# Kernel optimization log

Hardware: AMD Instinct MI355X
Metric: run time of the kernel (lower is better)

Reference implementation:

```python
import jax, jax.numpy as jnp
import numpy as np

N = 30000      # nodes
E = 480000     # edges (before self loops)
NFEAT = 128
H = 16         # heads
C = 32         # per-head channels = nhid
NCLASS = 10
G = 64         # graphs in batch
ATT_SLOPE = 0.2   # GATv2Conv negative_slope default
ACT_SLOPE = 0.01  # F.leaky_relu default


def setup_inputs() -> dict:
    key = jax.random.key(0)
    ks = jax.random.split(key, 16)
    def glorot(k, shape):
        fan = sum(shape[:2]) if len(shape) > 1 else shape[0]
        return jax.random.normal(k, shape, jnp.float32) * (2.0 / fan) ** 0.5
    inp = {
        "x": jax.random.normal(ks[0], (N, NFEAT), jnp.float32),
        # layer 1: lin_l / lin_r map NFEAT -> H*C, attention vector att [H, C]
        "Wl1": glorot(ks[1], (NFEAT, H * C)), "bl1": jnp.zeros((H * C,), jnp.float32),
        "Wr1": glorot(ks[2], (NFEAT, H * C)), "br1": jnp.zeros((H * C,), jnp.float32),
        "att1": glorot(ks[3], (H, C)), "b1": jnp.zeros((C,), jnp.float32),
        # layer 2: nhid(=C) -> H*C
        "Wl2": glorot(ks[4], (C, H * C)), "bl2": jnp.zeros((H * C,), jnp.float32),
        "Wr2": glorot(ks[5], (C, H * C)), "br2": jnp.zeros((H * C,), jnp.float32),
        "att2": glorot(ks[6], (H, C)), "b2": jnp.zeros((C,), jnp.float32),
        # classifier nhid -> nclass
        "Wc": glorot(ks[7], (C, NCLASS)), "bc": jnp.zeros((NCLASS,), jnp.float32),
        "edge_index": jax.random.randint(ks[8], (2, E), 0, N, jnp.int32),
        "batch": jnp.sort(jax.random.randint(ks[9], (N,), 0, G, jnp.int32)),
    }
    return inp


def _gatv2_layer(x, Wl, bl, Wr, br, att, b, src, dst, n):
    # GATv2Conv, concat=False (mean over heads), eval mode (no dropout)
    xl = (x @ Wl + bl).reshape(n, H, C)   # messages (x_j)
    xr = (x @ Wr + br).reshape(n, H, C)   # query side (x_i)
    e = jax.nn.leaky_relu(xl[src] + xr[dst], ATT_SLOPE)      # [E', H, C]
    score = jnp.einsum('ehc,hc->eh', e, att)                 # [E', H]
    # segment softmax over incoming edges of each dst node
    m = jax.ops.segment_max(score, dst, num_segments=n)
    ex = jnp.exp(score - m[dst])
    denom = jax.ops.segment_sum(ex, dst, num_segments=n)
    alpha = ex / denom[dst]                                  # [E', H]
    out = jax.ops.segment_sum(alpha[:, :, None] * xl[src], dst, num_segments=n)
    return out.mean(axis=1) + b                              # [n, C]


def reference(x, Wl1, bl1, Wr1, br1, att1, b1, Wl2, bl2, Wr2, br2, att2, b2, Wc, bc, edge_index, batch):
    # add self loops (PyG GATv2Conv default add_self_loops=True)
    loop = jnp.arange(N, dtype=edge_index.dtype)
    src = jnp.concatenate([edge_index[0], loop])
    dst = jnp.concatenate([edge_index[1], loop])

    h = jax.nn.leaky_relu(_gatv2_layer(x, Wl1, bl1, Wr1, br1, att1, b1, src, dst, N), ACT_SLOPE)
    h = jax.nn.leaky_relu(_gatv2_layer(h, Wl2, bl2, Wr2, br2, att2, b2, src, dst, N), ACT_SLOPE)
    # dropout is identity in eval mode
    # global mean pool over graphs
    summed = jax.ops.segment_sum(h, batch, num_segments=G)               # [G, C]
    counts = jax.ops.segment_sum(jnp.ones((N,), h.dtype), batch, num_segments=G)
    pooled = summed / jnp.maximum(counts, 1.0)[:, None]
    logits = pooled @ Wc + bc
    return logits / 1.0  # temperature = 1.0
```

## Files before the change

### kernel.cpp

```cpp
#include <hip/hip_runtime.h>
#include <float.h>

#define NNODES 30000
#define NEDGES 480000
#define NFEATK 128
#define NH 16
#define NC 32
#define HC 512
#define NCLASSES 10
#define NG 64
#define CAP 96

using half2v = __attribute__((ext_vector_type(2))) _Float16;
using half4 = __attribute__((ext_vector_type(4))) _Float16;
using half8 = __attribute__((ext_vector_type(8))) _Float16;
using f32x4 = __attribute__((ext_vector_type(4))) float;

__global__ void prep0_kernel(const float* __restrict__ x, _Float16* __restrict__ xh,
                             const float* __restrict__ Wl1, const float* __restrict__ Wr1,
                             _Float16* __restrict__ Wlt1, _Float16* __restrict__ Wrt1,
                             const float* __restrict__ Wl2, const float* __restrict__ Wr2,
                             _Float16* __restrict__ Wlt2, _Float16* __restrict__ Wrt2,
                             int* __restrict__ cnt, int* __restrict__ csr) {
    int gtid = blockIdx.x * blockDim.x + threadIdx.x;
    int gstride = gridDim.x * blockDim.x;
    for (int i = gtid; i < NNODES * NFEATK / 4; i += gstride) {
        float4 v = *(const float4*)&x[i * 4];
        half4 h = {(_Float16)v.x, (_Float16)v.y, (_Float16)v.z, (_Float16)v.w};
        *(half4*)&xh[i * 4] = h;
    }
    for (int i = gtid; i < 2 * 512 * NFEATK; i += gstride) {
        int sel = i >= 512 * NFEATK;
        int idx = i - sel * 512 * NFEATK;
        const float* W = sel ? Wr1 : Wl1;
        _Float16* Wt = sel ? Wrt1 : Wlt1;
        int n = idx & 511, k = idx >> 9;
        Wt[n * NFEATK + k] = (_Float16)W[idx];
    }
    for (int i = gtid; i < 2 * 512 * NC; i += gstride) {
        int sel = i >= 512 * NC;
        int idx = i - sel * 512 * NC;
        const float* W = sel ? Wr2 : Wl2;
        _Float16* Wt = sel ? Wrt2 : Wlt2;
        int n = idx & 511, k = idx >> 9;
        Wt[n * NC + k] = (_Float16)W[idx];
    }
    for (int i = gtid; i < NNODES; i += gstride) {
        cnt[i] = 1;
        csr[i * CAP] = i;
    }
}

__global__ void scatter_kernel(const int* __restrict__ src, const int* __restrict__ dst,
                               int* __restrict__ cnt, int* __restrict__ csr) {
    int e = blockIdx.x * blockDim.x + threadIdx.x;
    if (e >= NEDGES) return;
    int s = src[e], d = dst[e];
    int pos = atomicAdd(&cnt[d], 1);
    csr[d * CAP + pos] = s;
}

template <int K>
__launch_bounds__(256)
__global__ void dual_gemm_kernel(const _Float16* __restrict__ A,
                                 const _Float16* __restrict__ Wlt, const _Float16* __restrict__ Wrt,
                                 const float* __restrict__ bl, const float* __restrict__ br,
                                 _Float16* __restrict__ Yl, _Float16* __restrict__ Yr) {
    constexpr int Kc = K / 8;
    constexpr int AH = 64 * K;
    constexpr int BH = 128 * K;
    constexpr int YSH = 64 * 136;
    constexpr int SMEMH = (AH + BH > YSH) ? (AH + BH) : YSH;
    __shared__ __align__(16) _Float16 smem[SMEMH];
    _Float16* as = smem;
    _Float16* bs = smem + AH;

    int tid = threadIdx.x;
    int sel = blockIdx.y >> 2;
    int nbase = (blockIdx.y & 3) * 128;
    const _Float16* Bt = sel ? Wrt : Wlt;
    const float* bias = sel ? br : bl;
    _Float16* Y = sel ? Yr : Yl;
    int mb = blockIdx.x;

    for (int c = tid; c < 64 * Kc; c += 256) {
        int row = c / Kc, k8 = c % Kc;
        int arow = mb * 64 + row; if (arow > NNODES - 1) arow = NNODES - 1;
        half8 v = *(const half8*)&A[(size_t)arow * K + k8 * 8];
        *(half8*)&as[(row * Kc + (k8 ^ (row & (Kc - 1)))) * 8] = v;
    }
    for (int c = tid; c < 128 * Kc; c += 256) {
        int row = c / Kc, k8 = c % Kc;
        half8 v = *(const half8*)&Bt[(size_t)(nbase + row) * K + k8 * 8];
        *(half8*)&bs[(row * Kc + (k8 ^ (row & (Kc - 1)))) * 8] = v;
    }
    __syncthreads();

    int wave = tid >> 6, lane = tid & 63;
    int quad = lane >> 4, l16 = lane & 15;
    int am = l16 & (Kc - 1);

    f32x4 acc[8];
    #pragma unroll
    for (int f = 0; f < 8; f++) acc[f] = (f32x4){0.f, 0.f, 0.f, 0.f};

    #pragma unroll
    for (int kk = 0; kk < Kc; kk += 4) {
        int k8 = (kk + quad) ^ am;
        half8 a = *(const half8*)&as[((wave * 16 + l16) * Kc + k8) * 8];
        #pragma unroll
        for (int f = 0; f < 8; f++) {
            half8 b = *(const half8*)&bs[((f * 16 + l16) * Kc + k8) * 8];
            acc[f] = __builtin_amdgcn_mfma_f32_16x16x32_f16(a, b, acc[f], 0, 0, 0);
        }
    }
    __syncthreads();

    _Float16* ys = smem;
    #pragma unroll
    for (int f = 0; f < 8; f++) {
        float bv = bias[nbase + f * 16 + l16];
        #pragma unroll
        for (int r = 0; r < 4; r++) {
            ys[(wave * 16 + quad * 4 + r) * 136 + f * 16 + l16] = (_Float16)(acc[f][r] + bv);
        }
    }
    __syncthreads();
    int mtop = mb * 64;
    for (int c = tid; c < 64 * 16; c += 256) {
        int r = c >> 4, cc = (c & 15) * 8;
        int grow = mtop + r;
        if (grow < NNODES)
            *(half8*)&Y[(size_t)grow * HC + nbase + cc] = *(half8*)&ys[r * 136 + cc];
    }
}

__device__ inline half2v lrelu2(half2v e) {
    half2v s = e * half2v{(_Float16)0.2f, (_Float16)0.2f};
    return __builtin_elementwise_max(e, s);
}

#if __has_builtin(__builtin_amdgcn_fdot2)
#define FDOT2(a, b, c) __builtin_amdgcn_fdot2((a), (b), (c), false)
#else
__device__ inline float fdot2_sw(half2v a, half2v b, float c) {
    half2v p = a * b;
    return c + (float)p.x + (float)p.y;
}
#define FDOT2(a, b, c) fdot2_sw((a), (b), (c))
#endif

template <typename OUT>
__launch_bounds__(256)
__global__ void gat_edge_kernel(const _Float16* __restrict__ xlh, const _Float16* __restrict__ xrh,
                                const float* __restrict__ att, const float* __restrict__ bvec,
                                const int* __restrict__ cnt, const int* __restrict__ csr_src,
                                OUT* __restrict__ hout) {
    int wv = threadIdx.x >> 6;
    int t = threadIdx.x & 63;
    int d = blockIdx.x * 4 + wv;
    int col = t * 8;

    half8 xrq = *(const half8*)&xrh[(size_t)d * HC + col];
    half2v xr0 = {xrq[0], xrq[1]}, xr1 = {xrq[2], xrq[3]};
    half2v xr2 = {xrq[4], xrq[5]}, xr3 = {xrq[6], xrq[7]};
    float4 atta = *(const float4*)&att[col];
    float4 attb = *(const float4*)&att[col + 4];
    half2v at0 = {(_Float16)atta.x, (_Float16)atta.y};
    half2v at1 = {(_Float16)atta.z, (_Float16)atta.w};
    half2v at2 = {(_Float16)attb.x, (_Float16)attb.y};
    half2v at3 = {(_Float16)attb.z, (_Float16)attb.w};

    int beg = d * CAP, end = beg + cnt[d];

    float l = 0.f;
    float a[8];
    #pragma unroll
    for (int c = 0; c < 8; c++) a[c] = 0.f;

    for (int i = beg; i < end; i += 4) {
        int n = end - i;
        int s0 = csr_src[i];
        int s1 = csr_src[n > 1 ? i + 1 : i];
        int s2 = csr_src[n > 2 ? i + 2 : i];
        int s3 = csr_src[n > 3 ? i + 3 : i];
        half8 q0 = *(const half8*)&xlh[(size_t)s0 * HC + col];
        half8 q1 = *(const half8*)&xlh[(size_t)s1 * HC + col];
        half8 q2 = *(const half8*)&xlh[(size_t)s2 * HC + col];
        half8 q3 = *(const half8*)&xlh[(size_t)s3 * HC + col];

        float v0 = 0.f, v1 = 0.f, v2 = 0.f, v3 = 0.f;
        v0 = FDOT2(lrelu2(half2v{q0[0], q0[1]} + xr0), at0, v0);
        v0 = FDOT2(lrelu2(half2v{q0[2], q0[3]} + xr1), at1, v0);
        v0 = FDOT2(lrelu2(half2v{q0[4], q0[5]} + xr2), at2, v0);
        v0 = FDOT2(lrelu2(half2v{q0[6], q0[7]} + xr3), at3, v0);
        v1 = FDOT2(lrelu2(half2v{q1[0], q1[1]} + xr0), at0, v1);
        v1 = FDOT2(lrelu2(half2v{q1[2], q1[3]} + xr1), at1, v1);
        v1 = FDOT2(lrelu2(half2v{q1[4], q1[5]} + xr2), at2, v1);
        v1 = FDOT2(lrelu2(half2v{q1[6], q1[7]} + xr3), at3, v1);
        v2 = FDOT2(lrelu2(half2v{q2[0], q2[1]} + xr0), at0, v2);
        v2 = FDOT2(lrelu2(half2v{q2[2], q2[3]} + xr1), at1, v2);
        v2 = FDOT2(lrelu2(half2v{q2[4], q2[5]} + xr2), at2, v2);
        v2 = FDOT2(lrelu2(half2v{q2[6], q2[7]} + xr3), at3, v2);
        v3 = FDOT2(lrelu2(half2v{q3[0], q3[1]} + xr0), at0, v3);
        v3 = FDOT2(lrelu2(half2v{q3[2], q3[3]} + xr1), at1, v3);
        v3 = FDOT2(lrelu2(half2v{q3[4], q3[5]} + xr2), at2, v3);
        v3 = FDOT2(lrelu2(half2v{q3[6], q3[7]} + xr3), at3, v3);

        v0 += __shfl_xor(v0, 1); v1 += __shfl_xor(v1, 1);
        v2 += __shfl_xor(v2, 1); v3 += __shfl_xor(v3, 1);
        v0 += __shfl_xor(v0, 2); v1 += __shfl_xor(v1, 2);
        v2 += __shfl_xor(v2, 2); v3 += __shfl_xor(v3, 2);

        float p0 = __expf(v0);
        float p1 = (n > 1) ? __expf(v1) : 0.f;
        float p2 = (n > 2) ? __expf(v2) : 0.f;
        float p3 = (n > 3) ? __expf(v3) : 0.f;
        l += (p0 + p1) + (p2 + p3);

        #pragma unroll
        for (int c = 0; c < 8; c++) {
            a[c] += p0 * (float)q0[c];
            a[c] += p1 * (float)q1[c];
            a[c] += p2 * (float)q2[c];
            a[c] += p3 * (float)q3[c];
        }
    }

    float inv = 1.0f / l;
    #pragma unroll
    for (int c = 0; c < 8; c++) a[c] *= inv;

    #pragma unroll
    for (int off = 4; off < 64; off <<= 1) {
        #pragma unroll
        for (int c = 0; c < 8; c++) a[c] += __shfl_xor(a[c], off);
    }

    if (t < 4) {
        #pragma unroll
        for (int c = 0; c < 8; c++) {
            float r = a[c] * (1.0f / (float)NH) + bvec[t * 8 + c];
            r = (r > 0.f) ? r : 0.01f * r;
            hout[(size_t)d * NC + t * 8 + c] = (OUT)r;
        }
    }
}

__launch_bounds__(1024)
__global__ void pool_classify_kernel(const float* __restrict__ h, const int* __restrict__ batch,
                                     const float* __restrict__ Wc, const float* __restrict__ bc,
                                     float* __restrict__ out) {
    int g = blockIdx.x;
    int lo = 0, hi = NNODES;
    while (lo < hi) { int mid = (lo + hi) >> 1; if (batch[mid] < g) lo = mid + 1; else hi = mid; }
    int start = lo;
    hi = NNODES;
    while (lo < hi) { int mid = (lo + hi) >> 1; if (batch[mid] <= g) lo = mid + 1; else hi = mid; }
    int endn = lo;
    int cntg = endn - start;

    int tid = threadIdx.x;
    int c = tid & 31, nl = tid >> 5;
    float s = 0.f;
    for (int n = start + nl; n < endn; n += 32) s += h[n * NC + c];
    __shared__ float red[1024];
    red[tid] = s;
    __syncthreads();
    if (tid < 32) {
        float t = 0.f;
        #pragma unroll
        for (int j = 0; j < 32; j++) t += red[j * 32 + tid];
        red[tid] = t / fmaxf((float)cntg, 1.0f);
    }
    __syncthreads();
    if (tid < NCLASSES) {
        float sum = bc[tid];
        #pragma unroll
        for (int cc = 0; cc < NC; cc++) sum += red[cc] * Wc[cc * NCLASSES + tid];
        out[g * NCLASSES + tid] = sum;
    }
}


extern "C" void kernel_launch(void* const* d_in, const int* in_sizes, int n_in,
                              void* d_out, int out_size, void* d_ws, size_t ws_size,
                              hipStream_t stream) {
    const float* x    = (const float*)d_in[0];
    const float* Wl1  = (const float*)d_in[1];
    const float* bl1  = (const float*)d_in[2];
    const float* Wr1  = (const float*)d_in[3];
    const float* br1  = (const float*)d_in[4];
    const float* att1 = (const float*)d_in[5];
    const float* b1   = (const float*)d_in[6];
    const float* Wl2  = (const float*)d_in[7];
    const float* bl2  = (const float*)d_in[8];
    const float* Wr2  = (const float*)d_in[9];
    const float* br2  = (const float*)d_in[10];
    const float* att2 = (const float*)d_in[11];
    const float* b2   = (const float*)d_in[12];
    const float* Wc   = (const float*)d_in[13];
    const float* bc   = (const float*)d_in[14];
    const int* ei     = (const int*)d_in[15];
    const int* batch  = (const int*)d_in[16];
    float* out = (float*)d_out;

    const int* srcp = ei;
    const int* dstp = ei + NEDGES;

    char* ws = (char*)d_ws;
    size_t off = 0;
    auto alloc = [&](size_t bytes) -> void* {
        void* p = ws + off;
        off += (bytes + 255) & ~(size_t)255;
        return p;
    };
    _Float16* xlh  = (_Float16*)alloc(sizeof(_Float16) * (size_t)NNODES * HC);
    _Float16* xrh  = (_Float16*)alloc(sizeof(_Float16) * (size_t)NNODES * HC);
    _Float16* xh   = (_Float16*)alloc(sizeof(_Float16) * (size_t)NNODES * NFEATK);
    _Float16* h1   = (_Float16*)alloc(sizeof(_Float16) * (size_t)NNODES * NC);
    float* h2      = (float*)alloc(sizeof(float) * (size_t)NNODES * NC);
    _Float16* Wlt1 = (_Float16*)alloc(sizeof(_Float16) * 512 * NFEATK);
    _Float16* Wrt1 = (_Float16*)alloc(sizeof(_Float16) * 512 * NFEATK);
    _Float16* Wlt2 = (_Float16*)alloc(sizeof(_Float16) * 512 * NC);
    _Float16* Wrt2 = (_Float16*)alloc(sizeof(_Float16) * 512 * NC);
    int*   cnt     = (int*)alloc(sizeof(int) * NNODES);
    int*   csr     = (int*)alloc(sizeof(int) * (size_t)NNODES * CAP);

    prep0_kernel<<<512, 256, 0, stream>>>(x, xh, Wl1, Wr1, Wlt1, Wrt1,
                                          Wl2, Wr2, Wlt2, Wrt2, cnt, csr);
    scatter_kernel<<<(NEDGES + 255) / 256, 256, 0, stream>>>(srcp, dstp, cnt, csr);

    const int MB = (NNODES + 63) / 64;

    dual_gemm_kernel<NFEATK><<<dim3(MB, 8), 256, 0, stream>>>(xh, Wlt1, Wrt1, bl1, br1, xlh, xrh);
    gat_edge_kernel<_Float16><<<NNODES / 4, 256, 0, stream>>>(xlh, xrh, att1, b1, cnt, csr, h1);

    dual_gemm_kernel<NC><<<dim3(MB, 8), 256, 0, stream>>>(h1, Wlt2, Wrt2, bl2, br2, xlh, xrh);
    gat_edge_kernel<float><<<NNODES / 4, 256, 0, stream>>>(xlh, xrh, att2, b2, cnt, csr, h2);

    pool_classify_kernel<<<NG, 1024, 0, stream>>>(h2, batch, Wc, bc, out);
}
```

Measured before the change: 321.0 us.

## Split GAT edge aggregation across head slices with partial-sum reduce kernel

The edge kernel now splits each destination node's 16 heads into 8 slices of 2 heads, each handled by its own block. Within a wave, 8 edge slots are processed in parallel, one per group of 8 lanes, instead of one wave striding 4 edges over all 512 columns. Per-slice head sums go to a partial buffer, and a new head_reduce kernel adds the 8 slices, applies bias and leaky ReLU. This aims to raise parallelism and memory-level concurrency for low-degree nodes, at the cost of 8x more blocks, extra partial-buffer traffic and an extra launch per layer. Nontemporal loads and stores are also added.

```diff
diff --git a/kernel.cpp b/kernel.cpp
--- a/kernel.cpp
+++ b/kernel.cpp
@@ -10,6 +10,7 @@
 #define NCLASSES 10
 #define NG 64
 #define CAP 96
+#define NSLICE 8
 
 using half2v = __attribute__((ext_vector_type(2))) _Float16;
 using half4 = __attribute__((ext_vector_type(4))) _Float16;
@@ -150,100 +151,100 @@
 #define FDOT2(a, b, c) fdot2_sw((a), (b), (c))
 #endif
 
-template <typename OUT>
 __launch_bounds__(256)
 __global__ void gat_edge_kernel(const _Float16* __restrict__ xlh, const _Float16* __restrict__ xrh,
-                                const float* __restrict__ att, const float* __restrict__ bvec,
+                                const float* __restrict__ att,
                                 const int* __restrict__ cnt, const int* __restrict__ csr_src,
-                                OUT* __restrict__ hout) {
+                                float* __restrict__ part) {
+    int b = blockIdx.x;
+    int slice = b & 7;
     int wv = threadIdx.x >> 6;
     int t = threadIdx.x & 63;
-    int d = blockIdx.x * 4 + wv;
-    int col = t * 8;
-
-    half8 xrq = *(const half8*)&xrh[(size_t)d * HC + col];
+    int d = (b >> 3) * 4 + wv;
+    int slot = t >> 3;
+    int c8 = (t & 7) * 8;
+    int colbase = slice * 64;
+
+    half8 xrq = __builtin_nontemporal_load(
+        (const half8*)&xrh[(size_t)d * HC + colbase + c8]);
     half2v xr0 = {xrq[0], xrq[1]}, xr1 = {xrq[2], xrq[3]};
     half2v xr2 = {xrq[4], xrq[5]}, xr3 = {xrq[6], xrq[7]};
-    float4 atta = *(const float4*)&att[col];
-    float4 attb = *(const float4*)&att[col + 4];
+    float4 atta = *(const float4*)&att[colbase + c8];
+    float4 attb = *(const float4*)&att[colbase + c8 + 4];
     half2v at0 = {(_Float16)atta.x, (_Float16)atta.y};
     half2v at1 = {(_Float16)atta.z, (_Float16)atta.w};
     half2v at2 = {(_Float16)attb.x, (_Float16)attb.y};
     half2v at3 = {(_Float16)attb.z, (_Float16)attb.w};
 
-    int beg = d * CAP, end = beg + cnt[d];
+    int deg = __builtin_nontemporal_load(&cnt[d]);
+    int beg = d * CAP;
 
     float l = 0.f;
     float a[8];
     #pragma unroll
     for (int c = 0; c < 8; c++) a[c] = 0.f;
 
-    for (int i = beg; i < end; i += 4) {
-        int n = end - i;
-        int s0 = csr_src[i];
-        int s1 = csr_src[n > 1 ? i + 1 : i];
-        int s2 = csr_src[n > 2 ? i + 2 : i];
-        int s3 = csr_src[n > 3 ? i + 3 : i];
-        half8 q0 = *(const half8*)&xlh[(size_t)s0 * HC + col];
-        half8 q1 = *(const half8*)&xlh[(size_t)s1 * HC + col];
-        half8 q2 = *(const half8*)&xlh[(size_t)s2 * HC + col];
-        half8 q3 = *(const half8*)&xlh[(size_t)s3 * HC + col];
-
-        float v0 = 0.f, v1 = 0.f, v2 = 0.f, v3 = 0.f;
-        v0 = FDOT2(lrelu2(half2v{q0[0], q0[1]} + xr0), at0, v0);
-        v0 = FDOT2(lrelu2(half2v{q0[2], q0[3]} + xr1), at1, v0);
-        v0 = FDOT2(lrelu2(half2v{q0[4], q0[5]} + xr2), at2, v0);
-        v0 = FDOT2(lrelu2(half2v{q0[6], q0[7]} + xr3), at3, v0);
-        v1 = FDOT2(lrelu2(half2v{q1[0], q1[1]} + xr0), at0, v1);
-        v1 = FDOT2(lrelu2(half2v{q1[2], q1[3]} + xr1), at1, v1);
-        v1 = FDOT2(lrelu2(half2v{q1[4], q1[5]} + xr2), at2, v1);
-        v1 = FDOT2(lrelu2(half2v{q1[6], q1[7]} + xr3), at3, v1);
-        v2 = FDOT2(lrelu2(half2v{q2[0], q2[1]} + xr0), at0, v2);
-        v2 = FDOT2(lrelu2(half2v{q2[2], q2[3]} + xr1), at1, v2);
-        v2 = FDOT2(lrelu2(half2v{q2[4], q2[5]} + xr2), at2, v2);
-        v2 = FDOT2(lrelu2(half2v{q2[6], q2[7]} + xr3), at3, v2);
-        v3 = FDOT2(lrelu2(half2v{q3[0], q3[1]} + xr0), at0, v3);
-        v3 = FDOT2(lrelu2(half2v{q3[2], q3[3]} + xr1), at1, v3);
-        v3 = FDOT2(lrelu2(half2v{q3[4], q3[5]} + xr2), at2, v3);
-        v3 = FDOT2(lrelu2(half2v{q3[6], q3[7]} + xr3), at3, v3);
-
-        v0 += __shfl_xor(v0, 1); v1 += __shfl_xor(v1, 1);
-        v2 += __shfl_xor(v2, 1); v3 += __shfl_xor(v3, 1);
-        v0 += __shfl_xor(v0, 2); v1 += __shfl_xor(v1, 2);
-        v2 += __shfl_xor(v2, 2); v3 += __shfl_xor(v3, 2);
-
-        float p0 = __expf(v0);
-        float p1 = (n > 1) ? __expf(v1) : 0.f;
-        float p2 = (n > 2) ? __expf(v2) : 0.f;
-        float p3 = (n > 3) ? __expf(v3) : 0.f;
-        l += (p0 + p1) + (p2 + p3);
-
-        #pragma unroll
-        for (int c = 0; c < 8; c++) {
-            a[c] += p0 * (float)q0[c];
-            a[c] += p1 * (float)q1[c];
-            a[c] += p2 * (float)q2[c];
-            a[c] += p3 * (float)q3[c];
-        }
-    }
-
+    for (int it = 0; it < deg; it += 8) {
+        int e = it + slot;
+        int valid = e < deg;
+        int s = __builtin_nontemporal_load(&csr_src[beg + (valid ? e : 0)]);
+        half8 q = *(const half8*)&xlh[(size_t)s * HC + colbase + c8];
+
+        float v = 0.f;
+        v = FDOT2(lrelu2(half2v{q[0], q[1]} + xr0), at0, v);
+        v = FDOT2(lrelu2(half2v{q[2], q[3]} + xr1), at1, v);
+        v = FDOT2(lrelu2(half2v{q[4], q[5]} + xr2), at2, v);
+        v = FDOT2(lrelu2(half2v{q[6], q[7]} + xr3), at3, v);
+
+        v += __shfl_xor(v, 1);
+        v += __shfl_xor(v, 2);
+
+        float p = valid ? __expf(v) : 0.f;
+        l += p;
+        #pragma unroll
+        for (int c = 0; c < 8; c++) a[c] += p * (float)q[c];
+    }
+
+    #pragma unroll
+    for (int off = 8; off < 64; off <<= 1) {
+        l += __shfl_xor(l, off);
+        #pragma unroll
+        for (int c = 0; c < 8; c++) a[c] += __shfl_xor(a[c], off);
+    }
     float inv = 1.0f / l;
     #pragma unroll
     for (int c = 0; c < 8; c++) a[c] *= inv;
-
-    #pragma unroll
-    for (int off = 4; off < 64; off <<= 1) {
-        #pragma unroll
-        for (int c = 0; c < 8; c++) a[c] += __shfl_xor(a[c], off);
-    }
+    #pragma unroll
+    for (int c = 0; c < 8; c++) a[c] += __shfl_xor(a[c], 4);
 
     if (t < 4) {
-        #pragma unroll
-        for (int c = 0; c < 8; c++) {
-            float r = a[c] * (1.0f / (float)NH) + bvec[t * 8 + c];
-            r = (r > 0.f) ? r : 0.01f * r;
-            hout[(size_t)d * NC + t * 8 + c] = (OUT)r;
-        }
+        f32x4 o0 = {a[0], a[1], a[2], a[3]};
+        f32x4 o1 = {a[4], a[5], a[6], a[7]};
+        size_t o = ((size_t)slice * NNODES + d) * NC + t * 8;
+        __builtin_nontemporal_store(o0, (f32x4*)&part[o]);
+        __builtin_nontemporal_store(o1, (f32x4*)&part[o + 4]);
+    }
+}
+
+template <typename OUT>
+__launch_bounds__(256)
+__global__ void head_reduce_kernel(const float* __restrict__ part, const float* __restrict__ bvec,
+                                   OUT* __restrict__ hout) {
+    int i = blockIdx.x * blockDim.x + threadIdx.x;
+    if (i >= NNODES * (NC / 4)) return;
+    int d = i >> 3, c4 = (i & 7) * 4;
+    f32x4 s = {0.f, 0.f, 0.f, 0.f};
+    #pragma unroll
+    for (int sl = 0; sl < NSLICE; sl++) {
+        f32x4 v = *(const f32x4*)&part[((size_t)sl * NNODES + d) * NC + c4];
+        s += v;
+    }
+    const f32x4 bv = *(const f32x4*)&bvec[c4];
+    #pragma unroll
+    for (int j = 0; j < 4; j++) {
+        float r = s[j] * (1.0f / (float)NH) + bv[j];
+        r = (r > 0.f) ? r : 0.01f * r;
+        hout[(size_t)d * NC + c4 + j] = (OUT)r;
     }
 }
 
@@ -320,6 +321,7 @@
     _Float16* xh   = (_Float16*)alloc(sizeof(_Float16) * (size_t)NNODES * NFEATK);
     _Float16* h1   = (_Float16*)alloc(sizeof(_Float16) * (size_t)NNODES * NC);
     float* h2      = (float*)alloc(sizeof(float) * (size_t)NNODES * NC);
+    float* part    = (float*)alloc(sizeof(float) * (size_t)NSLICE * NNODES * NC);
     _Float16* Wlt1 = (_Float16*)alloc(sizeof(_Float16) * 512 * NFEATK);
     _Float16* Wrt1 = (_Float16*)alloc(sizeof(_Float16) * 512 * NFEATK);
     _Float16* Wlt2 = (_Float16*)alloc(sizeof(_Float16) * 512 * NC);
@@ -332,12 +334,16 @@
     scatter_kernel<<<(NEDGES + 255) / 256, 256, 0, stream>>>(srcp, dstp, cnt, csr);
 
     const int MB = (NNODES + 63) / 64;
+    const int EB = (NNODES / 4) * NSLICE;
+    const int RB = (NNODES * (NC / 4) + 255) / 256;
 
     dual_gemm_kernel<NFEATK><<<dim3(MB, 8), 256, 0, stream>>>(xh, Wlt1, Wrt1, bl1, br1, xlh, xrh);
-    gat_edge_kernel<_Float16><<<NNODES / 4, 256, 0, stream>>>(xlh, xrh, att1, b1, cnt, csr, h1);
+    gat_edge_kernel<<<EB, 256, 0, stream>>>(xlh, xrh, att1, cnt, csr, part);
+    head_reduce_kernel<_Float16><<<RB, 256, 0, stream>>>(part, b1, h1);
 
     dual_gemm_kernel<NC><<<dim3(MB, 8), 256, 0, stream>>>(h1, Wlt2, Wrt2, bl2, br2, xlh, xrh);
-    gat_edge_kernel<float><<<NNODES / 4, 256, 0, stream>>>(xlh, xrh, att2, b2, cnt, csr, h2);
+    gat_edge_kernel<<<EB, 256, 0, stream>>>(xlh, xrh, att2, cnt, csr, part);
+    head_reduce_kernel<float><<<RB, 256, 0, stream>>>(part, b2, h2);
 
     pool_classify_kernel<<<NG, 1024, 0, stream>>>(h2, batch, Wc, bc, out);
 }
```

New measurement: 482.3 us. +50.3%, slower.

## Bucket CSR neighbors by source range, store 16-bit indices, swap GEMM grid order

Applied to the files above, without the earlier changes.

CSR construction becomes count, scan and scatter passes. Within each destination's neighbor list, entries are grouped by source-node range (s>>11), which gives the gather in the edge kernel better locality into the source feature table. Indices are stored as 16-bit values, which shrinks the neighbor list, and address math uses 32-bit unsigned arithmetic. The GEMM grid is transposed so the eight column blocks that share each A tile run next to each other; the cost is two extra small kernel launches and a larger count array to zero.

```diff
diff --git a/kernel.cpp b/kernel.cpp
--- a/kernel.cpp
+++ b/kernel.cpp
@@ -10,6 +10,7 @@
 #define NCLASSES 10
 #define NG 64
 #define CAP 96
+#define NR 16
 
 using half2v = __attribute__((ext_vector_type(2))) _Float16;
 using half4 = __attribute__((ext_vector_type(4))) _Float16;
@@ -21,7 +22,7 @@
                              _Float16* __restrict__ Wlt1, _Float16* __restrict__ Wrt1,
                              const float* __restrict__ Wl2, const float* __restrict__ Wr2,
                              _Float16* __restrict__ Wlt2, _Float16* __restrict__ Wrt2,
-                             int* __restrict__ cnt, int* __restrict__ csr) {
+                             int* __restrict__ cnt16) {
     int gtid = blockIdx.x * blockDim.x + threadIdx.x;
     int gstride = gridDim.x * blockDim.x;
     for (int i = gtid; i < NNODES * NFEATK / 4; i += gstride) {
@@ -45,19 +46,42 @@
         int n = idx & 511, k = idx >> 9;
         Wt[n * NC + k] = (_Float16)W[idx];
     }
-    for (int i = gtid; i < NNODES; i += gstride) {
-        cnt[i] = 1;
-        csr[i * CAP] = i;
-    }
+    for (int i = gtid; i < NNODES * NR; i += gstride) cnt16[i] = 0;
+}
+
+__global__ void count_kernel(const int* __restrict__ src, const int* __restrict__ dst,
+                             int* __restrict__ cnt16) {
+    int i = blockIdx.x * blockDim.x + threadIdx.x;
+    if (i >= NEDGES + NNODES) return;
+    int s, d;
+    if (i < NEDGES) { s = src[i]; d = dst[i]; }
+    else            { d = i - NEDGES; s = d; }
+    atomicAdd(&cnt16[d * NR + (s >> 11)], 1);
+}
+
+__global__ void scan_kernel(const int* __restrict__ cnt16, int* __restrict__ cur16,
+                            int* __restrict__ cnt) {
+    int d = blockIdx.x * blockDim.x + threadIdx.x;
+    if (d >= NNODES) return;
+    int run = 0;
+    #pragma unroll
+    for (int r = 0; r < NR; r++) {
+        int c = cnt16[d * NR + r];
+        cur16[d * NR + r] = d * CAP + run;
+        run += c;
+    }
+    cnt[d] = run;
 }
 
 __global__ void scatter_kernel(const int* __restrict__ src, const int* __restrict__ dst,
-                               int* __restrict__ cnt, int* __restrict__ csr) {
-    int e = blockIdx.x * blockDim.x + threadIdx.x;
-    if (e >= NEDGES) return;
-    int s = src[e], d = dst[e];
-    int pos = atomicAdd(&cnt[d], 1);
-    csr[d * CAP + pos] = s;
+                               int* __restrict__ cur16, unsigned short* __restrict__ csr) {
+    int i = blockIdx.x * blockDim.x + threadIdx.x;
+    if (i >= NEDGES + NNODES) return;
+    int s, d;
+    if (i < NEDGES) { s = src[i]; d = dst[i]; }
+    else            { d = i - NEDGES; s = d; }
+    int pos = atomicAdd(&cur16[d * NR + (s >> 11)], 1);
+    csr[pos] = (unsigned short)s;
 }
 
 template <int K>
@@ -76,12 +100,12 @@
     _Float16* bs = smem + AH;
 
     int tid = threadIdx.x;
-    int sel = blockIdx.y >> 2;
-    int nbase = (blockIdx.y & 3) * 128;
+    int sel = blockIdx.x >> 2;
+    int nbase = (blockIdx.x & 3) * 128;
     const _Float16* Bt = sel ? Wrt : Wlt;
     const float* bias = sel ? br : bl;
     _Float16* Y = sel ? Yr : Yl;
-    int mb = blockIdx.x;
+    int mb = blockIdx.y;
 
     for (int c = tid; c < 64 * Kc; c += 256) {
         int row = c / Kc, k8 = c % Kc;
@@ -154,14 +178,14 @@
 __launch_bounds__(256)
 __global__ void gat_edge_kernel(const _Float16* __restrict__ xlh, const _Float16* __restrict__ xrh,
                                 const float* __restrict__ att, const float* __restrict__ bvec,
-                                const int* __restrict__ cnt, const int* __restrict__ csr_src,
+                                const int* __restrict__ cnt, const unsigned short* __restrict__ csr_src,
                                 OUT* __restrict__ hout) {
     int wv = threadIdx.x >> 6;
     int t = threadIdx.x & 63;
     int d = blockIdx.x * 4 + wv;
     int col = t * 8;
 
-    half8 xrq = *(const half8*)&xrh[(size_t)d * HC + col];
+    half8 xrq = *(const half8*)&xrh[(unsigned)d * HC + col];
     half2v xr0 = {xrq[0], xrq[1]}, xr1 = {xrq[2], xrq[3]};
     half2v xr2 = {xrq[4], xrq[5]}, xr3 = {xrq[6], xrq[7]};
     float4 atta = *(const float4*)&att[col];
@@ -184,10 +208,10 @@
         int s1 = csr_src[n > 1 ? i + 1 : i];
         int s2 = csr_src[n > 2 ? i + 2 : i];
         int s3 = csr_src[n > 3 ? i + 3 : i];
-        half8 q0 = *(const half8*)&xlh[(size_t)s0 * HC + col];
-        half8 q1 = *(const half8*)&xlh[(size_t)s1 * HC + col];
-        half8 q2 = *(const half8*)&xlh[(size_t)s2 * HC + col];
-        half8 q3 = *(const half8*)&xlh[(size_t)s3 * HC + col];
+        half8 q0 = *(const half8*)&xlh[(unsigned)s0 * HC + col];
+        half8 q1 = *(const half8*)&xlh[(unsigned)s1 * HC + col];
+        half8 q2 = *(const half8*)&xlh[(unsigned)s2 * HC + col];
+        half8 q3 = *(const half8*)&xlh[(unsigned)s3 * HC + col];
 
         float v0 = 0.f, v1 = 0.f, v2 = 0.f, v3 = 0.f;
         v0 = FDOT2(lrelu2(half2v{q0[0], q0[1]} + xr0), at0, v0);
@@ -325,18 +349,24 @@
     _Float16* Wlt2 = (_Float16*)alloc(sizeof(_Float16) * 512 * NC);
     _Float16* Wrt2 = (_Float16*)alloc(sizeof(_Float16) * 512 * NC);
     int*   cnt     = (int*)alloc(sizeof(int) * NNODES);
-    int*   csr     = (int*)alloc(sizeof(int) * (size_t)NNODES * CAP);
+    int*   cnt16   = (int*)alloc(sizeof(int) * (size_t)NNODES * NR);
+    int*   cur16   = (int*)alloc(sizeof(int) * (size_t)NNODES * NR);
+    unsigned short* csr = (unsigned short*)alloc(sizeof(unsigned short) * (size_t)NNODES * CAP);
+
+    const int EI = (NEDGES + NNODES + 255) / 256;
 
     prep0_kernel<<<512, 256, 0, stream>>>(x, xh, Wl1, Wr1, Wlt1, Wrt1,
-                                          Wl2, Wr2, Wlt2, Wrt2, cnt, csr);
-    scatter_kernel<<<(NEDGES + 255) / 256, 256, 0, stream>>>(srcp, dstp, cnt, csr);
+                                          Wl2, Wr2, Wlt2, Wrt2, cnt16);
+    count_kernel<<<EI, 256, 0, stream>>>(srcp, dstp, cnt16);
+    scan_kernel<<<(NNODES + 255) / 256, 256, 0, stream>>>(cnt16, cur16, cnt);
+    scatter_kernel<<<EI, 256, 0, stream>>>(srcp, dstp, cur16, csr);
 
     const int MB = (NNODES + 63) / 64;
 
-    dual_gemm_kernel<NFEATK><<<dim3(MB, 8), 256, 0, stream>>>(xh, Wlt1, Wrt1, bl1, br1, xlh, xrh);
+    dual_gemm_kernel<NFEATK><<<dim3(8, MB), 256, 0, stream>>>(xh, Wlt1, Wrt1, bl1, br1, xlh, xrh);
     gat_edge_kernel<_Float16><<<NNODES / 4, 256, 0, stream>>>(xlh, xrh, att1, b1, cnt, csr, h1);
 
-    dual_gemm_kernel<NC><<<dim3(MB, 8), 256, 0, stream>>>(h1, Wlt2, Wrt2, bl2, br2, xlh, xrh);
+    dual_gemm_kernel<NC><<<dim3(8, MB), 256, 0, stream>>>(h1, Wlt2, Wrt2, bl2, br2, xlh, xrh);
     gat_edge_kernel<float><<<NNODES / 4, 256, 0, stream>>>(xlh, xrh, att2, b2, cnt, csr, h2);
 
     pool_classify_kernel<<<NG, 1024, 0, stream>>>(h2, batch, Wc, bc, out);
```

Result: slower. 347.2 us (+8.2%).
